# Performance work log

Measured on AMD Instinct MI355X. Metric: run time of the kernel, lower is better.

Reference implementation:

```python
import jax, jax.numpy as jnp
import numpy as np
from jax import lax

K = 3      # kernel_size
PAD = 1    # padding
OG = 2     # offset groups


def _conv2d(x, w, b):
    y = lax.conv_general_dilated(x, w, (1, 1), [(PAD, PAD), (PAD, PAD)],
                                 dimension_numbers=('NCHW', 'OIHW', 'NCHW'))
    return y + b[None, :, None, None]


def _deform_conv2d(x, offset, mask, weight):
    # torchvision-style modulated deform_conv2d (v2), stride=1, dilation=1,
    # zero out-of-bounds, offset layout [B, OG*K*K*2, H, W] with (dy, dx) pairs.
    B, C, H, W = x.shape
    O = weight.shape[0]
    K2 = K * K
    Cg = C // OG

    ki, kj = jnp.meshgrid(jnp.arange(K), jnp.arange(K), indexing='ij')
    ki = ki.reshape(K2)
    kj = kj.reshape(K2)
    base_y = jnp.arange(H)[None, :] - PAD + ki[:, None]   # [K2, H]
    base_x = jnp.arange(W)[None, :] - PAD + kj[:, None]   # [K2, W]

    off = offset.reshape(B, OG, K2, 2, H, W)
    py = off[:, :, :, 0] + base_y[None, None, :, :, None].astype(x.dtype)  # [B,OG,K2,H,W]
    px = off[:, :, :, 1] + base_x[None, None, :, None, :].astype(x.dtype)
    m = mask.reshape(B, OG, K2, H, W)

    y0f = jnp.floor(py)
    x0f = jnp.floor(px)
    wy1 = py - y0f   # bilinear weights, grads flow through py/px
    wx1 = px - x0f
    y0 = y0f.astype(jnp.int32)
    x0 = x0f.astype(jnp.int32)
    y1 = y0 + 1
    x1 = x0 + 1

    img = x.reshape(B, OG, Cg, H * W)

    def gather(yi, xi):
        valid = (yi >= 0) & (yi < H) & (xi >= 0) & (xi < W)
        idx = jnp.clip(yi, 0, H - 1) * W + jnp.clip(xi, 0, W - 1)          # [B,OG,K2,H,W]
        v = jnp.take_along_axis(img[:, :, :, None, :],
                                idx.reshape(B, OG, 1, K2, H * W), axis=-1)
        return v.reshape(B, OG, Cg, K2, H, W) * valid[:, :, None].astype(x.dtype)

    v00 = gather(y0, x0)
    v01 = gather(y0, x1)
    v10 = gather(y1, x0)
    v11 = gather(y1, x1)

    wy1e = wy1[:, :, None]   # [B,OG,1,K2,H,W]
    wx1e = wx1[:, :, None]
    val = (v00 * (1 - wy1e) * (1 - wx1e)
           + v01 * (1 - wy1e) * wx1e
           + v10 * wy1e * (1 - wx1e)
           + v11 * wy1e * wx1e)
    val = val * m[:, :, None]                               # modulation mask

    wr = weight.reshape(O, OG, Cg, K2)
    return jnp.einsum('ogck,bgckhw->bohw', wr, val)


def setup_inputs() -> dict:
    key = jax.random.key(0)
    k1, k2, k3, k4, k5 = jax.random.split(key, 5)
    B, C, O, H, W = 4, 64, 64, 128, 128
    K2 = K * K
    x = jax.random.normal(k1, (B, C, H, W), dtype=jnp.float32)
    w_main = jax.random.normal(k2, (O, C, K, K), dtype=jnp.float32) / np.sqrt(C * K2)
    w_off = jax.random.normal(k3, (2 * OG * K2, C, K, K), dtype=jnp.float32) * 0.01
    b_off = jax.random.normal(k4, (2 * OG * K2,), dtype=jnp.float32) * 0.01
    w_mask = jnp.full((OG * K2, C, K, K), 0.5, dtype=jnp.float32)  # init_mask = 0.5
    b_mask = jax.random.normal(k5, (OG * K2,), dtype=jnp.float32) * 0.01
    return {"x": x, "w_main": w_main, "w_off": w_off, "b_off": b_off,
            "w_mask": w_mask, "b_mask": b_mask}


def reference(x, w_main, w_off, b_off, w_mask, b_mask):
    offset = _conv2d(x, w_off, b_off)
    mask = jax.nn.sigmoid(_conv2d(x, w_mask, b_mask))
    return _deform_conv2d(x, offset, mask, w_main)
```

## Files before the change

kernel.cpp:

```cpp
#include <hip/hip_runtime.h>
#include <math.h>

#define BB 4
#define C 64
#define O 64
#define H 128
#define W 128
#define K2 9
#define HW (H*W)
#define NOFF 36
#define NMSK 18

typedef __bf16 bf16;
typedef bf16 bf16x8 __attribute__((ext_vector_type(8)));
typedef float f32x4 __attribute__((ext_vector_type(4)));
typedef unsigned short u16x4 __attribute__((ext_vector_type(4)));

#define BSTR 60
#define VAL_BYTES 20480
#define SMEM_BYTES 35840
#define NW_TOTAL 73728
#define WFRAG 18432

__device__ inline unsigned short f2h_bits(float f) {
  _Float16 h = (_Float16)f;
  return __builtin_bit_cast(unsigned short, h);
}
__device__ inline float h2f(unsigned short u) {
  return (float)__builtin_bit_cast(_Float16, u);
}

__global__ __launch_bounds__(256) void prep_all(
    const float* __restrict__ x, const float* __restrict__ w_main,
    const float* __restrict__ w_off, const float* __restrict__ w_mask,
    unsigned short* __restrict__ xT16, bf16* __restrict__ wfC,
    bf16* __restrict__ wfM) {
  __shared__ float tile[64][65];
  int tid = threadIdx.x;
  int b = blockIdx.x >> 8;
  int p0 = (blockIdx.x & 255) * 64;
#pragma unroll
  for (int it = 0; it < 16; ++it) {
    int c = it * 4 + (tid >> 6);
    tile[c][tid & 63] = x[(size_t)(b * C + c) * HW + p0 + (tid & 63)];
  }
  __syncthreads();
#pragma unroll
  for (int it = 0; it < 4; ++it) {
    int p = it * 16 + (tid >> 4);
    int cq = tid & 15;
    u16x4 o;
#pragma unroll
    for (int j = 0; j < 4; ++j) {
      bf16 t = (bf16)tile[cq * 4 + j][p];
      o[j] = __builtin_bit_cast(unsigned short, t);
    }
    *(u16x4*)&xT16[(size_t)(b * HW + p0 + p) * C + cq * 4] = o;
  }
  int i = blockIdx.x * 256 + tid;
  if (i < NW_TOTAL) {
    int which = (i >= 36864);
    int ii = which ? i - 36864 : i;
    int j = ii & 7;
    int l = (ii >> 3) & 63;
    int rest = ii >> 9;
    int to = rest & 3;
    int kk = (rest >> 2) % 9;
    int ph = (rest >> 2) / 9;
    int m = to * 16 + (l & 15);
    int u = kk * 32 + (l >> 4) * 8 + j;
    int tap = u >> 5;
    int c1 = u & 31;
    if (!which) {
      int c = ph * 32 + c1;
      float v = (m < NOFF) ? w_off[(m * C + c) * K2 + tap]
                : (m < 54) ? w_mask[((m - NOFF) * C + c) * K2 + tap]
                           : 0.f;
      wfC[ii] = (bf16)v;
    } else {
      wfM[ii] = (bf16)w_main[(m * C + ph * 32 + c1) * K2 + tap];
    }
  }
}

template <int KK0, int NKK>
__device__ inline void mfma_chunk(const bf16* __restrict__ wb,
                                  const bf16* __restrict__ val, int row,
                                  int q4, int lane, f32x4* acc) {
#pragma unroll
  for (int t = 0; t < NKK; ++t) {
    int kk = KK0 + t;
    bf16x8 bfr = *(const bf16x8*)(val + ((t * 64 + row) * 32 + q4 * 8));
#pragma unroll
    for (int to = 0; to < 4; ++to) {
      bf16x8 afr = *(const bf16x8*)(wb + (size_t)((kk * 4 + to) * 64 + lane) * 8);
      acc[to] = __builtin_amdgcn_mfma_f32_16x16x32_bf16(afr, bfr, acc[to], 0, 0, 0);
    }
  }
}

__global__ __launch_bounds__(256, 4) void fused_deform(
    const bf16* __restrict__ xT, const bf16* __restrict__ wfC,
    const bf16* __restrict__ wfM, const float* __restrict__ b_off,
    const float* __restrict__ b_mask, float* __restrict__ out) {
  __shared__ __align__(16) char smem[SMEM_BYTES];
  bf16* val = (bf16*)smem;
  unsigned int (*buf)[BSTR] = (unsigned int (*)[BSTR])(smem + VAL_BYTES);
  float* bufF = (float*)(smem + VAL_BYTES);
  bf16x8* stage16 = (bf16x8*)(smem + VAL_BYTES);
  float* valF = (float*)smem;

  const int tid = threadIdx.x;
  const int lane = tid & 63;
  const int wv = tid >> 6;
  const int n16 = lane & 15;
  const int q4 = lane >> 4;
  const int chunk = tid & 3;
  const int pg = tid >> 2;
  const int row = wv * 16 + n16;

  const int b = blockIdx.x >> 8;
  const int ti = blockIdx.x & 255;
  const int h0 = ti >> 1;
  const int w0 = (ti & 1) * 64;
  const bf16* xb = xT + (size_t)b * HW * C;

  bf16x8 zero8;
#pragma unroll
  for (int j = 0; j < 8; ++j) zero8[j] = (bf16)0.f;

  f32x4 accC[4] = {{0.f,0.f,0.f,0.f},{0.f,0.f,0.f,0.f},
                   {0.f,0.f,0.f,0.f},{0.f,0.f,0.f,0.f}};
#pragma unroll 1
  for (int ph = 0; ph < 2; ++ph) {
    if (ph) __syncthreads();
#pragma unroll
    for (int it = 0; it < 4; ++it) {
      int id = it * 256 + tid;
      if (id < 816) {
        int q2 = id & 3;
        int wp = (id >> 2) % 68;
        int r = (id >> 2) / 68;
        int yy = h0 + r - 1;
        int xx = w0 + wp - 1;
        bf16x8 v = zero8;
        if ((unsigned)yy < (unsigned)H && (unsigned)xx < (unsigned)W)
          v = *(const bf16x8*)(xb + (size_t)((yy << 7) + xx) * C + ph * 32 + q2 * 8);
        stage16[id] = v;
      }
    }
    __syncthreads();
#pragma unroll
    for (int t = 0; t < 5; ++t) {
      int tap = t;
      bf16x8 v = stage16[((tap / 3) * 68 + pg + tap % 3) * 4 + chunk];
      *(bf16x8*)(val + ((t * 64 + pg) * 32 + chunk * 8)) = v;
    }
    __syncthreads();
    mfma_chunk<0, 5>(wfC + (size_t)ph * WFRAG, val, row, q4, lane, accC);
    __syncthreads();
#pragma unroll
    for (int t = 0; t < 4; ++t) {
      int tap = 5 + t;
      bf16x8 v = stage16[((tap / 3) * 68 + pg + tap % 3) * 4 + chunk];
      *(bf16x8*)(val + ((t * 64 + pg) * 32 + chunk * 8)) = v;
    }
    __syncthreads();
    mfma_chunk<5, 4>(wfC + (size_t)ph * WFRAG, val, row, q4, lane, accC);
  }
  {
#pragma unroll
    for (int to = 0; to < 4; ++to)
#pragma unroll
      for (int r = 0; r < 4; ++r) {
        int o = to * 16 + q4 * 4 + r;
        float a = accC[to][r];
        if (o < NOFF) {
          bufF[row * BSTR + o] = a + b_off[o];
        } else if (o < 54) {
          float s = a + b_mask[o - NOFF];
          bufF[row * BSTR + o] = 1.f / (1.f + __expf(-s));
        }
      }
  }
  __syncthreads();

  unsigned int rW0[5], rW1[5], rCo[5];
#pragma unroll
  for (int it = 0; it < 5; ++it) {
    int t = it * 256 + tid;
    if (t < 1152) {
      int p = t & 63;
      int gk = t >> 6;
      int g = gk / 9, tap = gk % 9;
      float offy = bufF[p * BSTR + 2 * gk];
      float offx = bufF[p * BSTR + 2 * gk + 1];
      float m = bufF[p * BSTR + NOFF + gk];
      float py = offy + (float)(h0 + tap / 3 - 1);
      float px = offx + (float)(w0 + p + tap % 3 - 1);
      float y0f = floorf(py), x0f = floorf(px);
      float wy1 = py - y0f, wx1 = px - x0f;
      float wy0 = 1.f - wy1, wx0 = 1.f - wx1;
      int y0 = (int)y0f, x0 = (int)x0f;
      int y1 = y0 + 1, x1 = x0 + 1;
      bool y0ok = (unsigned)y0 < (unsigned)H, y1ok = (unsigned)y1 < (unsigned)H;
      bool x0ok = (unsigned)x0 < (unsigned)W, x1ok = (unsigned)x1 < (unsigned)W;
      float w00 = (y0ok && x0ok) ? wy0 * wx0 * m : 0.f;
      float w01 = (y0ok && x1ok) ? wy0 * wx1 * m : 0.f;
      float w10 = (y1ok && x0ok) ? wy1 * wx0 * m : 0.f;
      float w11 = (y1ok && x1ok) ? wy1 * wx1 * m : 0.f;
      unsigned int y0c = (unsigned)min(max(y0, 0), H - 1);
      unsigned int y1c = (unsigned)min(max(y1, 0), H - 1);
      unsigned int x0c = (unsigned)min(max(x0, 0), W - 1);
      unsigned int x1c = (unsigned)min(max(x1, 0), W - 1);
      rW0[it] = (unsigned)f2h_bits(w00) | ((unsigned)f2h_bits(w01) << 16);
      rW1[it] = (unsigned)f2h_bits(w10) | ((unsigned)f2h_bits(w11) << 16);
      rCo[it] = y0c | (x0c << 8) | (y1c << 16) | (x1c << 24);
    }
  }
  __syncthreads();
#pragma unroll
  for (int it = 0; it < 5; ++it) {
    int t = it * 256 + tid;
    if (t < 1152) {
      int p = t & 63;
      int gk = t >> 6;
      buf[p][2 * gk] = rW0[it];
      buf[p][2 * gk + 1] = rW1[it];
      buf[p][NOFF + gk] = rCo[it];
    }
  }
  __syncthreads();

  f32x4 accM[4] = {{0.f,0.f,0.f,0.f},{0.f,0.f,0.f,0.f},
                   {0.f,0.f,0.f,0.f},{0.f,0.f,0.f,0.f}};
#pragma unroll 1
  for (int g = 0; g < 2; ++g) {
    if (g) __syncthreads();
    const bf16* bb = xb + g * 32 + chunk * 8;
#pragma unroll 1
    for (int kc = 0; kc < 2; ++kc) {
      int tap0 = kc ? 5 : 0;
      int ntap = kc ? 4 : 5;
      if (kc) __syncthreads();
#pragma unroll 5
      for (int t = 0; t < ntap; ++t) {
        int tap = tap0 + t;
        int gk = g * 9 + tap;
        unsigned int wab = buf[pg][2 * gk];
        unsigned int wcd = buf[pg][2 * gk + 1];
        unsigned int pk = buf[pg][NOFF + gk];
        float w00 = h2f(wab & 0xffff), w01 = h2f(wab >> 16);
        float w10 = h2f(wcd & 0xffff), w11 = h2f(wcd >> 16);
        int r0 = (int)(pk & 255) << 7;
        int x0 = (int)((pk >> 8) & 255);
        int r1 = (int)((pk >> 16) & 255) << 7;
        int x1 = (int)(pk >> 24);
        bf16x8 v00 = *(const bf16x8*)(bb + (size_t)(r0 + x0) * C);
        bf16x8 v01 = *(const bf16x8*)(bb + (size_t)(r0 + x1) * C);
        bf16x8 v10 = *(const bf16x8*)(bb + (size_t)(r1 + x0) * C);
        bf16x8 v11 = *(const bf16x8*)(bb + (size_t)(r1 + x1) * C);
        bf16x8 res;
#pragma unroll
        for (int j = 0; j < 8; ++j) {
          float v = (float)v00[j] * w00 + (float)v01[j] * w01 +
                    (float)v10[j] * w10 + (float)v11[j] * w11;
          res[j] = (bf16)v;
        }
        *(bf16x8*)(val + ((t * 64 + pg) * 32 + chunk * 8)) = res;
      }
      __syncthreads();
      if (kc)
        mfma_chunk<5, 4>(wfM + (size_t)g * WFRAG, val, row, q4, lane, accM);
      else
        mfma_chunk<0, 5>(wfM + (size_t)g * WFRAG, val, row, q4, lane, accM);
    }
  }

  __syncthreads();
  {
#pragma unroll
    for (int to = 0; to < 4; ++to)
#pragma unroll
      for (int r = 0; r < 4; ++r)
        valF[(to * 16 + q4 * 4 + r) * 68 + row] = accM[to][r];
  }
  __syncthreads();
  {
    float* ob = out + (size_t)b * O * HW + (h0 << 7) + w0;
#pragma unroll
    for (int it = 0; it < 4; ++it) {
      int id = it * 256 + tid;
      int o = id >> 4, seg = id & 15;
      f32x4 v = *(f32x4*)&valF[o * 68 + seg * 4];
      *(f32x4*)&ob[(size_t)o * HW + seg * 4] = v;
    }
  }
}

extern "C" void kernel_launch(void* const* d_in, const int* in_sizes, int n_in,
                              void* d_out, int out_size, void* d_ws,
                              size_t ws_size, hipStream_t stream) {
  const float* x = (const float*)d_in[0];
  const float* w_main = (const float*)d_in[1];
  const float* w_off = (const float*)d_in[2];
  const float* b_off = (const float*)d_in[3];
  const float* w_mask = (const float*)d_in[4];
  const float* b_mask = (const float*)d_in[5];
  float* out = (float*)d_out;

  unsigned short* xT16 = (unsigned short*)d_ws;
  bf16* wfC = (bf16*)(xT16 + (size_t)BB * HW * C);
  bf16* wfM = wfC + 36864;

  prep_all<<<1024, 256, 0, stream>>>(x, w_main, w_off, w_mask, xT16, wfC, wfM);
  fused_deform<<<1024, 256, 0, stream>>>((const bf16*)xT16, wfC, wfM, b_off,
                                         b_mask, out);
}
```

Measured before the change: 123.5 us.

## Shrink LDS footprint, read offset-conv operands directly from staging, raise occupancy

The offset/mask convolution now feeds MFMA B-fragments straight from the staged halo tile instead of copying each tap into a separate val buffer, which removes several copy passes and barriers. The main deformable GEMM is split into three chunks of three taps, so the val buffer shrinks and the buffer stride drops. Together these lower shared memory per block so launch bounds can target six blocks per CU. Blocks are remapped so neighbouring block IDs cover different images/halves, and the prep transpose uses vectorized 128-bit loads and 8-wide stores. Risks include register pressure at the higher occupancy target and extra barriers from the three-chunk loop.

```diff
diff --git a/kernel.cpp b/kernel.cpp
--- a/kernel.cpp
+++ b/kernel.cpp
@@ -9,18 +9,18 @@
 #define K2 9
 #define HW (H*W)
 #define NOFF 36
-#define NMSK 18
 
 typedef __bf16 bf16;
 typedef bf16 bf16x8 __attribute__((ext_vector_type(8)));
 typedef float f32x4 __attribute__((ext_vector_type(4)));
-typedef unsigned short u16x4 __attribute__((ext_vector_type(4)));
-
-#define BSTR 60
-#define VAL_BYTES 20480
-#define SMEM_BYTES 35840
+typedef unsigned short u16x8 __attribute__((ext_vector_type(8)));
+
+#define BSTR 55
+#define VAL_BYTES 12288
+#define BUF_BYTES (64*BSTR*4)
+#define SMEM_BYTES (VAL_BYTES + BUF_BYTES)
+#define WFRAG 18432
 #define NW_TOTAL 73728
-#define WFRAG 18432
 
 __device__ inline unsigned short f2h_bits(float f) {
   _Float16 h = (_Float16)f;
@@ -35,27 +35,30 @@
     const float* __restrict__ w_off, const float* __restrict__ w_mask,
     unsigned short* __restrict__ xT16, bf16* __restrict__ wfC,
     bf16* __restrict__ wfM) {
-  __shared__ float tile[64][65];
+  __shared__ float tile[64][68];
   int tid = threadIdx.x;
   int b = blockIdx.x >> 8;
   int p0 = (blockIdx.x & 255) * 64;
 #pragma unroll
-  for (int it = 0; it < 16; ++it) {
-    int c = it * 4 + (tid >> 6);
-    tile[c][tid & 63] = x[(size_t)(b * C + c) * HW + p0 + (tid & 63)];
-  }
-  __syncthreads();
-#pragma unroll
   for (int it = 0; it < 4; ++it) {
-    int p = it * 16 + (tid >> 4);
-    int cq = tid & 15;
-    u16x4 o;
-#pragma unroll
-    for (int j = 0; j < 4; ++j) {
-      bf16 t = (bf16)tile[cq * 4 + j][p];
-      o[j] = __builtin_bit_cast(unsigned short, t);
-    }
-    *(u16x4*)&xT16[(size_t)(b * HW + p0 + p) * C + cq * 4] = o;
+    int c = it * 16 + (tid >> 4);
+    int p4 = (tid & 15) * 4;
+    *(f32x4*)&tile[c][p4] =
+        *(const f32x4*)(x + (size_t)(b * C + c) * HW + p0 + p4);
+  }
+  __syncthreads();
+#pragma unroll
+  for (int it = 0; it < 2; ++it) {
+    int t = it * 256 + tid;
+    int p = t >> 3;
+    int h8 = t & 7;
+    u16x8 o;
+#pragma unroll
+    for (int j = 0; j < 8; ++j) {
+      bf16 v = (bf16)tile[h8 * 8 + j][p];
+      o[j] = __builtin_bit_cast(unsigned short, v);
+    }
+    *(u16x8*)&xT16[(size_t)(b * HW + p0 + p) * C + h8 * 8] = o;
   }
   int i = blockIdx.x * 256 + tid;
   if (i < NW_TOTAL) {
@@ -83,23 +86,7 @@
   }
 }
 
-template <int KK0, int NKK>
-__device__ inline void mfma_chunk(const bf16* __restrict__ wb,
-                                  const bf16* __restrict__ val, int row,
-                                  int q4, int lane, f32x4* acc) {
-#pragma unroll
-  for (int t = 0; t < NKK; ++t) {
-    int kk = KK0 + t;
-    bf16x8 bfr = *(const bf16x8*)(val + ((t * 64 + row) * 32 + q4 * 8));
-#pragma unroll
-    for (int to = 0; to < 4; ++to) {
-      bf16x8 afr = *(const bf16x8*)(wb + (size_t)((kk * 4 + to) * 64 + lane) * 8);
-      acc[to] = __builtin_amdgcn_mfma_f32_16x16x32_bf16(afr, bfr, acc[to], 0, 0, 0);
-    }
-  }
-}
-
-__global__ __launch_bounds__(256, 4) void fused_deform(
+__global__ __launch_bounds__(256, 6) void fused_deform(
     const bf16* __restrict__ xT, const bf16* __restrict__ wfC,
     const bf16* __restrict__ wfM, const float* __restrict__ b_off,
     const float* __restrict__ b_mask, float* __restrict__ out) {
@@ -108,6 +95,7 @@
   unsigned int (*buf)[BSTR] = (unsigned int (*)[BSTR])(smem + VAL_BYTES);
   float* bufF = (float*)(smem + VAL_BYTES);
   bf16x8* stage16 = (bf16x8*)(smem + VAL_BYTES);
+  const bf16* stageb = (const bf16*)(smem + VAL_BYTES);
   float* valF = (float*)smem;
 
   const int tid = threadIdx.x;
@@ -119,8 +107,10 @@
   const int pg = tid >> 2;
   const int row = wv * 16 + n16;
 
-  const int b = blockIdx.x >> 8;
-  const int ti = blockIdx.x & 255;
+  const int g8 = blockIdx.x & 7;
+  const int slot = blockIdx.x >> 3;
+  const int b = g8 >> 1;
+  const int ti = (g8 & 1) * 128 + slot;
   const int h0 = ti >> 1;
   const int w0 = (ti & 1) * 64;
   const bf16* xb = xT + (size_t)b * HW * C;
@@ -150,24 +140,20 @@
       }
     }
     __syncthreads();
-#pragma unroll
-    for (int t = 0; t < 5; ++t) {
-      int tap = t;
-      bf16x8 v = stage16[((tap / 3) * 68 + pg + tap % 3) * 4 + chunk];
-      *(bf16x8*)(val + ((t * 64 + pg) * 32 + chunk * 8)) = v;
-    }
-    __syncthreads();
-    mfma_chunk<0, 5>(wfC + (size_t)ph * WFRAG, val, row, q4, lane, accC);
-    __syncthreads();
-#pragma unroll
-    for (int t = 0; t < 4; ++t) {
-      int tap = 5 + t;
-      bf16x8 v = stage16[((tap / 3) * 68 + pg + tap % 3) * 4 + chunk];
-      *(bf16x8*)(val + ((t * 64 + pg) * 32 + chunk * 8)) = v;
-    }
-    __syncthreads();
-    mfma_chunk<5, 4>(wfC + (size_t)ph * WFRAG, val, row, q4, lane, accC);
-  }
+    const bf16* wb = wfC + (size_t)ph * WFRAG;
+#pragma unroll
+    for (int kk = 0; kk < 9; ++kk) {
+      bf16x8 bfr = *(const bf16x8*)(stageb +
+          (size_t)(((kk / 3) * 68 + row + kk % 3) * 4 + q4) * 8);
+#pragma unroll
+      for (int to = 0; to < 4; ++to) {
+        bf16x8 afr = *(const bf16x8*)(wb + (size_t)((kk * 4 + to) * 64 + lane) * 8);
+        accC[to] = __builtin_amdgcn_mfma_f32_16x16x32_bf16(afr, bfr, accC[to], 0, 0, 0);
+      }
+    }
+  }
+  __syncthreads();
+
   {
 #pragma unroll
     for (int to = 0; to < 4; ++to)
@@ -236,16 +222,13 @@
                    {0.f,0.f,0.f,0.f},{0.f,0.f,0.f,0.f}};
 #pragma unroll 1
   for (int g = 0; g < 2; ++g) {
-    if (g) __syncthreads();
     const bf16* bb = xb + g * 32 + chunk * 8;
 #pragma unroll 1
-    for (int kc = 0; kc < 2; ++kc) {
-      int tap0 = kc ? 5 : 0;
-      int ntap = kc ? 4 : 5;
-      if (kc) __syncthreads();
-#pragma unroll 5
-      for (int t = 0; t < ntap; ++t) {
-        int tap = tap0 + t;
+    for (int kc = 0; kc < 3; ++kc) {
+      if (g || kc) __syncthreads();
+#pragma unroll
+      for (int t = 0; t < 3; ++t) {
+        int tap = kc * 3 + t;
         int gk = g * 9 + tap;
         unsigned int wab = buf[pg][2 * gk];
         unsigned int wcd = buf[pg][2 * gk + 1];
@@ -270,10 +253,17 @@
         *(bf16x8*)(val + ((t * 64 + pg) * 32 + chunk * 8)) = res;
       }
       __syncthreads();
-      if (kc)
-        mfma_chunk<5, 4>(wfM + (size_t)g * WFRAG, val, row, q4, lane, accM);
-      else
-        mfma_chunk<0, 5>(wfM + (size_t)g * WFRAG, val, row, q4, lane, accM);
+      const bf16* wb = wfM + (size_t)g * WFRAG;
+#pragma unroll
+      for (int t = 0; t < 3; ++t) {
+        int kk = kc * 3 + t;
+        bf16x8 bfr = *(const bf16x8*)(val + ((t * 64 + row) * 32 + q4 * 8));
+#pragma unroll
+        for (int to = 0; to < 4; ++to) {
+          bf16x8 afr = *(const bf16x8*)(wb + (size_t)((kk * 4 + to) * 64 + lane) * 8);
+          accM[to] = __builtin_amdgcn_mfma_f32_16x16x32_bf16(afr, bfr, accM[to], 0, 0, 0);
+        }
+      }
     }
   }
 
```

After: 116.9 us. 1.06x faster.
